# Kernel optimization log

Measured on AMD Instinct MI355X. Metric: run time of the kernel, lower is better.

Reference implementation:

```python
import jax, jax.numpy as jnp
import numpy as np

N, E, B = 51200, 819200, 64
F, G, GH, LH, LOUT = 64, 64, 128, 128, 1


def setup_inputs() -> dict:
    key = jax.random.key(0)
    ks = jax.random.split(key, 10)
    x = jax.random.normal(ks[0], (N, F), dtype=jnp.float32)
    e = jax.random.uniform(ks[1], (N, 1), dtype=jnp.float32)  # data.p[:, 0].view(-1, 1)
    edge_index = jax.random.randint(ks[2], (2, E), 0, N, dtype=jnp.int64)
    batch = jnp.sort(jax.random.randint(ks[3], (N,), 0, B, dtype=jnp.int64))

    def init_w(k, fan_in, fan_out):
        return (jax.random.normal(k, (fan_in, fan_out), dtype=jnp.float32)
                / np.float32(np.sqrt(fan_in)))

    # global PTConv nn: MLP(2F -> GH -> G)
    gW1 = init_w(ks[4], 2 * F, GH)
    gb1 = jnp.zeros((GH,), dtype=jnp.float32)
    gW2 = init_w(ks[5], GH, G)
    gb2 = jnp.zeros((G,), dtype=jnp.float32)
    # local PTConv nn: MLP(2*(F+G) -> LH -> 1)
    lW1 = init_w(ks[6], 2 * (F + G), LH)
    lb1 = jnp.zeros((LH,), dtype=jnp.float32)
    lW2 = init_w(ks[7], LH, LOUT)
    lb2 = jnp.zeros((LOUT,), dtype=jnp.float32)
    return {"x": x, "e": e, "edge_index": edge_index, "batch": batch,
            "gW1": gW1, "gb1": gb1, "gW2": gW2, "gb2": gb2,
            "lW1": lW1, "lb1": lb1, "lW2": lW2, "lb2": lb2}


def _mlp(h, W1, b1, W2, b2):
    return jax.nn.relu(h @ W1 + b1) @ W2 + b2


def _ptconv(x, edge_index, W1, b1, W2, b2, num_nodes):
    # PyG convention: edge_index[0]=src (j), edge_index[1]=dst (i); aggr='add'
    src, dst = edge_index[0], edge_index[1]
    h = jnp.concatenate([x[dst], x[src]], axis=-1)  # [E, 2*Fin] edge gather
    m = _mlp(h, W1, b1, W2, b2)                      # [E, Fout] edge MLP
    return jax.ops.segment_sum(m, dst, num_segments=num_nodes)  # scatter-add


def reference(x, e, edge_index, batch,
              gW1, gb1, gW2, gb2, lW1, lb1, lW2, lb2):
    n = x.shape[0]
    # EFNGlobal: PTConv -> energy weighting -> global_add_pool
    g = _ptconv(x, edge_index, gW1, gb1, gW2, gb2, n)   # [N, G]
    g = e * g                                           # e = p[:, 0:1]
    pooled = jax.ops.segment_sum(g, batch, num_segments=B)  # [B, G]
    # EFNLocal: broadcast per-graph scalars to nodes, concat, PTConv
    scalars = pooled[batch]                             # [N, G]
    xl = jnp.concatenate([x, scalars], axis=-1)         # [N, F+G]
    w_i = _ptconv(xl, edge_index, lW1, lb1, lW2, lb2, n)  # [N, 1]
    return w_i
```

## Files before the change

### kernel.cpp

```cpp
#include <hip/hip_runtime.h>
#include <hip/hip_bf16.h>

#define NN 51200
#define EE 819200
#define BB 64
#define NS 32
#define NPWG 4
#define NPWL 4
#define NBUCK 512
#define NPB 100
#define CAP 4096
#define EPB 4096

typedef __attribute__((ext_vector_type(8))) short short8;
typedef __attribute__((ext_vector_type(4))) float f32x4;

__device__ __forceinline__ ushort f2bf(float f) {
    unsigned int u = __float_as_uint(f);
    unsigned int r = (u + 0x7FFFu + ((u >> 16) & 1u)) >> 16;
    return (ushort)r;
}
__device__ __forceinline__ unsigned int cvt_pk_bf16(float lo, float hi) {
    unsigned int r;
    asm("v_cvt_pk_bf16_f32 %0, %1, %2" : "=v"(r) : "v"(lo), "v"(hi));
    return r;
}

__global__ void prep_weights(const float* __restrict__ gW1, const float* __restrict__ lW1,
                             ushort* __restrict__ W1p, ushort* __restrict__ L1p) {
    int tid = threadIdx.x;
    for (int idx = tid; idx < 64 * 256; idx += 512) {
        int i = idx & 7, c = (idx >> 3) & 255, q = idx >> 11;
        int k = (q >> 2) * 32 + (q & 3) * 8 + i;
        W1p[idx] = f2bf(c < 128 ? gW1[k * 128 + c] : gW1[(64 + k) * 128 + (c - 128)]);
        L1p[idx] = f2bf(c < 128 ? lW1[k * 128 + c] : lW1[(128 + k) * 128 + (c - 128)]);
    }
}

__global__ __launch_bounds__(512) void bucketA_kernel(const int* __restrict__ eidx,
                                                      int* __restrict__ bcnt,
                                                      int2* __restrict__ btmp) {
    __shared__ int2 sp[EPB];
    __shared__ ushort sb[EPB];
    __shared__ ushort perm[EPB];
    __shared__ int cnts[NBUCK];
    __shared__ int lofs[NBUCK];
    __shared__ int lcur[NBUCK];
    __shared__ int gbase[NBUCK];
    const int tid = threadIdx.x;
    const int base = blockIdx.x * EPB;

    cnts[tid] = 0;
    __syncthreads();
    for (int i = tid; i < EPB; i += 512) {
        int d = eidx[EE + base + i], s = eidx[base + i];
        sp[i] = make_int2(s, d);
        int b = d / NPB;
        sb[i] = (ushort)b;
        atomicAdd(&cnts[b], 1);
    }
    __syncthreads();
    const int v = cnts[tid];
    lofs[tid] = v;
    __syncthreads();
    for (int o = 1; o < NBUCK; o <<= 1) {
        int u = (tid >= o) ? lofs[tid - o] : 0;
        __syncthreads();
        lofs[tid] += u;
        __syncthreads();
    }
    const int excl = lofs[tid] - v;
    lofs[tid] = excl;
    lcur[tid] = excl;
    gbase[tid] = (v > 0) ? atomicAdd(&bcnt[tid * 16], v) : 0;
    __syncthreads();
    for (int i = tid; i < EPB; i += 512) {
        int pos = atomicAdd(&lcur[sb[i]], 1);
        perm[pos] = (ushort)i;
    }
    __syncthreads();
    {
        const int c = cnts[tid];
        const int lo = lofs[tid];
        int2* dst = btmp + (long)tid * CAP + gbase[tid];
        for (int j = 0; j < c; ++j) dst[j] = sp[perm[lo + j]];
    }
}

__global__ __launch_bounds__(512) void bucket_scan_kernel(const int* __restrict__ bcnt,
                                                          int* __restrict__ bbase) {
    __shared__ int s[NBUCK];
    const int t = threadIdx.x;
    int v = bcnt[t * 16];
    s[t] = v;
    __syncthreads();
    for (int o = 1; o < NBUCK; o <<= 1) {
        int u = (t >= o) ? s[t - o] : 0;
        __syncthreads();
        s[t] += u;
        __syncthreads();
    }
    bbase[t] = s[t] - v;
}

__global__ __launch_bounds__(256) void bucketB_kernel(const int2* __restrict__ btmp,
                                                      const int* __restrict__ bcnt,
                                                      const int* __restrict__ bbase,
                                                      int* __restrict__ offs,
                                                      int* __restrict__ csr) {
    __shared__ int lcnt[NPB];
    __shared__ int lofs[NPB];
    __shared__ int lcur[NPB];
    __shared__ int2 pairs[2048];
    const int bkt = blockIdx.x, tid = threadIdx.x;
    const int cnt = bcnt[bkt * 16];
    const int base = bbase[bkt];
    for (int j = tid; j < NPB; j += 256) lcnt[j] = 0;
    __syncthreads();
    for (int i = tid; i < cnt; i += 256) {
        int2 p = btmp[(long)bkt * CAP + i];
        if (i < 2048) pairs[i] = p;
        atomicAdd(&lcnt[p.y - bkt * NPB], 1);
    }
    __syncthreads();
    if (tid == 0) {
        int run = base;
        for (int j = 0; j < NPB; ++j) { lofs[j] = run; run += lcnt[j]; }
    }
    __syncthreads();
    for (int j = tid; j < NPB; j += 256) {
        lcur[j] = lofs[j];
        offs[bkt * NPB + j] = lofs[j];
    }
    if (bkt == NBUCK - 1 && tid == 0) offs[NN] = EE;
    __syncthreads();
    for (int i = tid; i < cnt; i += 256) {
        int2 p = (i < 2048) ? pairs[i] : btmp[(long)bkt * CAP + i];
        int pos = atomicAdd(&lcur[p.y - bkt * NPB], 1);
        csr[pos] = p.x;
    }
}

__global__ __launch_bounds__(512) void pq_gemm(
        const float* __restrict__ x, const ushort* __restrict__ Wp,
        const float* __restrict__ bias1, const float* __restrict__ T12,
        const int* __restrict__ batch, ushort* __restrict__ out) {
    const int tid = threadIdx.x;
    const int w = tid >> 6, l = tid & 63, lr = l & 15, lg = l >> 4;
    const int node = blockIdx.x * 128 + w * 16 + lr;

    short8 xa[2];
#pragma unroll
    for (int ks = 0; ks < 2; ++ks) {
        const float4* bp = reinterpret_cast<const float4*>(x + (long)node * 64 + ks * 32 + lg * 8);
        float4 f0 = bp[0], f1 = bp[1];
        union { short8 s; unsigned int u[4]; } t;
        t.u[0] = cvt_pk_bf16(f0.x, f0.y);
        t.u[1] = cvt_pk_bf16(f0.z, f0.w);
        t.u[2] = cvt_pk_bf16(f1.x, f1.y);
        t.u[3] = cvt_pk_bf16(f1.z, f1.w);
        xa[ks] = t.s;
    }
    f32x4 acc[16];
#pragma unroll
    for (int t = 0; t < 16; ++t)
#pragma unroll
        for (int i = 0; i < 4; ++i)
            acc[t][i] = (t < 8) ? bias1[t * 16 + lg * 4 + i] : 0.f;
#pragma unroll
    for (int ks = 0; ks < 2; ++ks)
#pragma unroll
        for (int t = 0; t < 16; ++t) {
            short8 wf = *reinterpret_cast<const short8*>(Wp + (((ks * 4 + lg) * 256) + t * 16 + lr) * 8);
            acc[t] = __builtin_amdgcn_mfma_f32_16x16x32_bf16(wf, xa[ks], acc[t], 0, 0, 0);
        }
    if (T12) {
        const float* tp = T12 + (long)batch[node] * 256;
#pragma unroll
        for (int t = 0; t < 16; ++t)
#pragma unroll
            for (int i = 0; i < 4; ++i)
                acc[t][i] += tp[t * 16 + lg * 4 + i];
    }
#pragma unroll
    for (int t = 0; t < 16; ++t) {
        uint2 v;
        v.x = cvt_pk_bf16(acc[t][0], acc[t][1]);
        v.y = cvt_pk_bf16(acc[t][2], acc[t][3]);
        *reinterpret_cast<uint2*>(out + (long)node * 256 + t * 16 + lg * 4) = v;
    }
}

__global__ __launch_bounds__(256) void global_edge(
        const ushort* __restrict__ PQ, const int* __restrict__ csr,
        const int* __restrict__ offs, const float* __restrict__ e,
        const int* __restrict__ batch,
        float* __restrict__ hidpart, float* __restrict__ esumpart) {
    const int tid = threadIdx.x;
    const int w = tid >> 6, l = tid & 63;
    const int wid = blockIdx.x * 4 + w;
    const int node0 = __builtin_amdgcn_readfirstlane(wid * NPWG);
    const int slot = wid & (NS - 1);

    float accp0 = 0.f, accp1 = 0.f, eacc = 0.f;
    int curb = batch[node0];

    for (int n = 0; n < NPWG; ++n) {
        const int node = node0 + n;
        const int off  = offs[node];
        const int cnt  = offs[node + 1] - off;
        const int bb   = batch[node];
        const float ev = e[node];
        if (bb != curb) {
            float* hp = hidpart + (long)slot * (BB * 128) + curb * 128;
            atomicAdd(hp + 2 * l, accp0);
            atomicAdd(hp + 2 * l + 1, accp1);
            if (l == 0) atomicAdd(&esumpart[slot * BB + curb], eacc);
            accp0 = accp1 = eacc = 0.f;
            curb = bb;
        }
        if (cnt <= 0) continue;
        const unsigned int pdu = *reinterpret_cast<const unsigned int*>(PQ + (long)node * 256 + 2 * l);
        const float p0 = __uint_as_float(pdu << 16);
        const float p1 = __uint_as_float(pdu & 0xFFFF0000u);
        float h0 = 0.f, h1 = 0.f;
        int g = 0;
        for (; g + 8 <= cnt; g += 8) {
            unsigned int qv[8];
#pragma unroll
            for (int k = 0; k < 8; ++k) {
                const int s = csr[off + g + k];
                qv[k] = *reinterpret_cast<const unsigned int*>(PQ + (long)s * 256 + 128 + 2 * l);
            }
#pragma unroll
            for (int k = 0; k < 8; ++k) {
                h0 += fmaxf(p0 + __uint_as_float(qv[k] << 16), 0.f);
                h1 += fmaxf(p1 + __uint_as_float(qv[k] & 0xFFFF0000u), 0.f);
            }
        }
        for (; g < cnt; ++g) {
            const int s = csr[off + g];
            const unsigned int qv = *reinterpret_cast<const unsigned int*>(PQ + (long)s * 256 + 128 + 2 * l);
            h0 += fmaxf(p0 + __uint_as_float(qv << 16), 0.f);
            h1 += fmaxf(p1 + __uint_as_float(qv & 0xFFFF0000u), 0.f);
        }
        accp0 += ev * h0; accp1 += ev * h1; eacc += ev * (float)cnt;
    }
    {
        float* hp = hidpart + (long)slot * (BB * 128) + curb * 128;
        atomicAdd(hp + 2 * l, accp0);
        atomicAdd(hp + 2 * l + 1, accp1);
        if (l == 0) atomicAdd(&esumpart[slot * BB + curb], eacc);
    }
}

__global__ __launch_bounds__(256) void pooled_t12_kernel(
        const float* __restrict__ hidpart, const float* __restrict__ esumpart,
        const float* __restrict__ gW2, const float* __restrict__ gb2,
        const float* __restrict__ lW1, float* __restrict__ T12) {
    __shared__ float hs[128];
    __shared__ float qacc[4][64];
    __shared__ float pb[64];
    __shared__ float esv;
    const int b = blockIdx.x, tid = threadIdx.x;
    if (tid < 128) {
        float s = 0.f;
        for (int sl = 0; sl < NS; ++sl) s += hidpart[(long)sl * (BB * 128) + b * 128 + tid];
        hs[tid] = s;
    } else if (tid == 128) {
        float s = 0.f;
        for (int sl = 0; sl < NS; ++sl) s += esumpart[sl * BB + b];
        esv = s;
    }
    __syncthreads();
    {
        int col = tid & 63, qr = tid >> 6;
        float a = 0.f;
        for (int k = qr * 32; k < qr * 32 + 32; ++k) a += hs[k] * gW2[k * 64 + col];
        qacc[qr][col] = a;
    }
    __syncthreads();
    if (tid < 64) pb[tid] = qacc[0][tid] + qacc[1][tid] + qacc[2][tid] + qacc[3][tid] + esv * gb2[tid];
    __syncthreads();
    const float* col = (tid < 128) ? (lW1 + 64 * 128 + tid) : (lW1 + 192 * 128 + (tid - 128));
    float acc = 0.f;
    for (int k = 0; k < 64; ++k) acc += pb[k] * col[k * 128];
    T12[b * 256 + tid] = acc;
}

__global__ __launch_bounds__(256) void local_edge(
        const ushort* __restrict__ PQL, const int* __restrict__ csr,
        const int* __restrict__ offs, const float* __restrict__ lW2,
        const float* __restrict__ lb2, float* __restrict__ out) {
    const int tid = threadIdx.x;
    const int w = tid >> 6, l = tid & 63;
    const int wid = blockIdx.x * 4 + w;
    const int node0 = __builtin_amdgcn_readfirstlane(wid * NPWL);
    const float w20 = lW2[2 * l], w21 = lW2[2 * l + 1];
    const float b2v = lb2[0];

    for (int n = 0; n < NPWL; ++n) {
        const int node = node0 + n;
        const int off = offs[node];
        const int cnt = offs[node + 1] - off;
        float dacc = 0.f;
        if (cnt > 0) {
            const unsigned int pdu = *reinterpret_cast<const unsigned int*>(PQL + (long)node * 256 + 2 * l);
            const float p0 = __uint_as_float(pdu << 16);
            const float p1 = __uint_as_float(pdu & 0xFFFF0000u);
            int g = 0;
            for (; g + 8 <= cnt; g += 8) {
                unsigned int qv[8];
#pragma unroll
                for (int k = 0; k < 8; ++k) {
                    const int s = csr[off + g + k];
                    qv[k] = *reinterpret_cast<const unsigned int*>(PQL + (long)s * 256 + 128 + 2 * l);
                }
#pragma unroll
                for (int k = 0; k < 8; ++k) {
                    dacc += fmaxf(p0 + __uint_as_float(qv[k] << 16), 0.f) * w20
                          + fmaxf(p1 + __uint_as_float(qv[k] & 0xFFFF0000u), 0.f) * w21;
                }
            }
            for (; g < cnt; ++g) {
                const int s = csr[off + g];
                const unsigned int qv = *reinterpret_cast<const unsigned int*>(PQL + (long)s * 256 + 128 + 2 * l);
                dacc += fmaxf(p0 + __uint_as_float(qv << 16), 0.f) * w20
                      + fmaxf(p1 + __uint_as_float(qv & 0xFFFF0000u), 0.f) * w21;
            }
            dacc += __shfl_xor(dacc, 1, 64);
            dacc += __shfl_xor(dacc, 2, 64);
            dacc += __shfl_xor(dacc, 4, 64);
            dacc += __shfl_xor(dacc, 8, 64);
            dacc += __shfl_xor(dacc, 16, 64);
            dacc += __shfl_xor(dacc, 32, 64);
        }
        if (l == 0) out[node] = dacc + (float)cnt * b2v;
    }
}

extern "C" void kernel_launch(void* const* d_in, const int* in_sizes, int n_in,
                              void* d_out, int out_size, void* d_ws, size_t ws_size,
                              hipStream_t stream) {
    const float* x   = (const float*)d_in[0];
    const float* e   = (const float*)d_in[1];
    const int*   ei  = (const int*)d_in[2];
    const int*   bat = (const int*)d_in[3];
    const float* gW1 = (const float*)d_in[4];
    const float* gb1 = (const float*)d_in[5];
    const float* gW2 = (const float*)d_in[6];
    const float* gb2 = (const float*)d_in[7];
    const float* lW1 = (const float*)d_in[8];
    const float* lb1 = (const float*)d_in[9];
    const float* lW2 = (const float*)d_in[10];
    const float* lb2 = (const float*)d_in[11];

    char* ws = (char*)d_ws;
    ushort* W1p     = (ushort*)(ws);
    ushort* L1p     = (ushort*)(ws + 32768);
    float*  T12     = (float*)(ws + 65536);
    float*  esumpart= (float*)(ws + 131072);
    float*  hidpart = (float*)(ws + 139264);
    int*    offs    = (int*)(ws + 1187840);
    int*    bcnt    = (int*)(ws + 1392672);
    int*    bbase   = (int*)(ws + 1425440);
    int*    csr     = (int*)(ws + 1427488);
    ushort* PQ      = (ushort*)(ws + 4704288);
    int2*   btmp    = (int2*)PQ;

    hipMemsetAsync(bcnt, 0, 32768, stream);
    hipMemsetAsync(esumpart, 0, 8192 + 1048576, stream);
    hipMemsetAsync(d_out, 0, (size_t)out_size * sizeof(float), stream);

    prep_weights<<<1, 512, 0, stream>>>(gW1, lW1, W1p, L1p);
    bucketA_kernel<<<EE / EPB, 512, 0, stream>>>(ei, bcnt, btmp);
    bucket_scan_kernel<<<1, NBUCK, 0, stream>>>(bcnt, bbase);
    bucketB_kernel<<<NBUCK, 256, 0, stream>>>(btmp, bcnt, bbase, offs, csr);

    pq_gemm<<<NN / 128, 512, 0, stream>>>(x, W1p, gb1, nullptr, bat, PQ);
    global_edge<<<NN / (4 * NPWG), 256, 0, stream>>>(PQ, csr, offs, e, bat, hidpart, esumpart);
    pooled_t12_kernel<<<BB, 256, 0, stream>>>(hidpart, esumpart, gW2, gb2, lW1, T12);
    pq_gemm<<<NN / 128, 512, 0, stream>>>(x, L1p, lb1, T12, bat, PQ);
    local_edge<<<NN / (4 * NPWL), 256, 0, stream>>>(PQ, csr, offs, lW2, lb2, (float*)d_out);
}
```

Before: 180.8 us.

## Partition CSR by source range and process edge ranges per 16-node group

The CSR build now also splits each destination bucket into four source-node ranges, producing a per-range offset table, and packs the local destination index into the upper bits of each CSR entry. Edge kernels launch one block per source range and node group and stream a contiguous edge range, switching destination on the fly and accumulating outputs with atomics. The goal is better cache locality for the gathered source rows (each block touches only a quarter of PQ) and even load balance across waves. The cost is extra atomics on outputs, per-edge branch checks, and a larger scan.

```diff
diff --git a/kernel.cpp b/kernel.cpp
--- a/kernel.cpp
+++ b/kernel.cpp
@@ -5,8 +5,8 @@
 #define EE 819200
 #define BB 64
 #define NS 32
-#define NPWG 4
-#define NPWL 4
+#define R4 4
+#define RSIZE 12800
 #define NBUCK 512
 #define NPB 100
 #define CAP 4096
@@ -25,6 +25,8 @@
     asm("v_cvt_pk_bf16_f32 %0, %1, %2" : "=v"(r) : "v"(lo), "v"(hi));
     return r;
 }
+__device__ __forceinline__ float blo(unsigned int q) { return __uint_as_float(q << 16); }
+__device__ __forceinline__ float bhi(unsigned int q) { return __uint_as_float(q & 0xFFFF0000u); }
 
 __global__ void prep_weights(const float* __restrict__ gW1, const float* __restrict__ lW1,
                              ushort* __restrict__ W1p, ushort* __restrict__ L1p) {
@@ -39,27 +41,28 @@
 
 __global__ __launch_bounds__(512) void bucketA_kernel(const int* __restrict__ eidx,
                                                       int* __restrict__ bcnt,
+                                                      int* __restrict__ cnt4,
                                                       int2* __restrict__ btmp) {
     __shared__ int2 sp[EPB];
-    __shared__ ushort sb[EPB];
     __shared__ ushort perm[EPB];
-    __shared__ int cnts[NBUCK];
-    __shared__ int lofs[NBUCK];
-    __shared__ int lcur[NBUCK];
-    __shared__ int gbase[NBUCK];
+    __shared__ int cnts[NBUCK], lofs[NBUCK], lcur[NBUCK];
+    __shared__ int c4[R4 * NBUCK];
     const int tid = threadIdx.x;
     const int base = blockIdx.x * EPB;
 
     cnts[tid] = 0;
+#pragma unroll
+    for (int j = 0; j < 4; ++j) c4[tid + j * 512] = 0;
     __syncthreads();
     for (int i = tid; i < EPB; i += 512) {
         int d = eidx[EE + base + i], s = eidx[base + i];
         sp[i] = make_int2(s, d);
-        int b = d / NPB;
-        sb[i] = (ushort)b;
-        atomicAdd(&cnts[b], 1);
-    }
-    __syncthreads();
+        atomicAdd(&cnts[d / NPB], 1);
+        atomicAdd(&c4[(s / RSIZE) * NBUCK + d / NPB], 1);
+    }
+    __syncthreads();
+    for (int j = tid; j < R4 * NBUCK; j += 512)
+        if (c4[j]) atomicAdd(&cnt4[j], c4[j]);
     const int v = cnts[tid];
     lofs[tid] = v;
     __syncthreads();
@@ -72,72 +75,77 @@
     const int excl = lofs[tid] - v;
     lofs[tid] = excl;
     lcur[tid] = excl;
-    gbase[tid] = (v > 0) ? atomicAdd(&bcnt[tid * 16], v) : 0;
+    const int mygbase = (v > 0) ? atomicAdd(&bcnt[tid * 16], v) : 0;
     __syncthreads();
     for (int i = tid; i < EPB; i += 512) {
-        int pos = atomicAdd(&lcur[sb[i]], 1);
+        int pos = atomicAdd(&lcur[sp[i].y / NPB], 1);
         perm[pos] = (ushort)i;
     }
     __syncthreads();
     {
         const int c = cnts[tid];
         const int lo = lofs[tid];
-        int2* dst = btmp + (long)tid * CAP + gbase[tid];
+        int2* dst = btmp + (long)tid * CAP + mygbase;
         for (int j = 0; j < c; ++j) dst[j] = sp[perm[lo + j]];
     }
 }
 
-__global__ __launch_bounds__(512) void bucket_scan_kernel(const int* __restrict__ bcnt,
-                                                          int* __restrict__ bbase) {
-    __shared__ int s[NBUCK];
+__global__ __launch_bounds__(512) void scan2048_kernel(const int* __restrict__ cnt4,
+                                                       int* __restrict__ base4,
+                                                       int* __restrict__ roffs4) {
+    __shared__ int s[512];
     const int t = threadIdx.x;
-    int v = bcnt[t * 16];
-    s[t] = v;
-    __syncthreads();
-    for (int o = 1; o < NBUCK; o <<= 1) {
+    int v0 = cnt4[t * 4], v1 = cnt4[t * 4 + 1], v2 = cnt4[t * 4 + 2], v3 = cnt4[t * 4 + 3];
+    int sum = v0 + v1 + v2 + v3;
+    s[t] = sum;
+    __syncthreads();
+    for (int o = 1; o < 512; o <<= 1) {
         int u = (t >= o) ? s[t - o] : 0;
         __syncthreads();
         s[t] += u;
         __syncthreads();
     }
-    bbase[t] = s[t] - v;
+    int run = s[t] - sum;
+    base4[t * 4] = run;
+    base4[t * 4 + 1] = run + v0;
+    base4[t * 4 + 2] = run + v0 + v1;
+    base4[t * 4 + 3] = run + v0 + v1 + v2;
+    if (t == 0) roffs4[R4 * NN] = EE;
 }
 
 __global__ __launch_bounds__(256) void bucketB_kernel(const int2* __restrict__ btmp,
                                                       const int* __restrict__ bcnt,
-                                                      const int* __restrict__ bbase,
-                                                      int* __restrict__ offs,
+                                                      const int* __restrict__ base4,
+                                                      int* __restrict__ roffs4,
                                                       int* __restrict__ csr) {
-    __shared__ int lcnt[NPB];
-    __shared__ int lofs[NPB];
-    __shared__ int lcur[NPB];
+    __shared__ int lcnt[R4 * NPB];
+    __shared__ int lcur[R4 * NPB];
     __shared__ int2 pairs[2048];
     const int bkt = blockIdx.x, tid = threadIdx.x;
     const int cnt = bcnt[bkt * 16];
-    const int base = bbase[bkt];
-    for (int j = tid; j < NPB; j += 256) lcnt[j] = 0;
+    for (int j = tid; j < R4 * NPB; j += 256) lcnt[j] = 0;
     __syncthreads();
     for (int i = tid; i < cnt; i += 256) {
         int2 p = btmp[(long)bkt * CAP + i];
         if (i < 2048) pairs[i] = p;
-        atomicAdd(&lcnt[p.y - bkt * NPB], 1);
-    }
-    __syncthreads();
-    if (tid == 0) {
-        int run = base;
-        for (int j = 0; j < NPB; ++j) { lofs[j] = run; run += lcnt[j]; }
-    }
-    __syncthreads();
-    for (int j = tid; j < NPB; j += 256) {
-        lcur[j] = lofs[j];
-        offs[bkt * NPB + j] = lofs[j];
-    }
-    if (bkt == NBUCK - 1 && tid == 0) offs[NN] = EE;
+        int key = (p.x / RSIZE) * NPB + (p.y - bkt * NPB);
+        atomicAdd(&lcnt[key], 1);
+    }
+    __syncthreads();
+    if (tid < R4) {
+        int run = base4[tid * NBUCK + bkt];
+        for (int nl = 0; nl < NPB; ++nl) {
+            roffs4[tid * NN + bkt * NPB + nl] = run;
+            lcur[tid * NPB + nl] = run;
+            run += lcnt[tid * NPB + nl];
+        }
+    }
     __syncthreads();
     for (int i = tid; i < cnt; i += 256) {
         int2 p = (i < 2048) ? pairs[i] : btmp[(long)bkt * CAP + i];
-        int pos = atomicAdd(&lcur[p.y - bkt * NPB], 1);
-        csr[pos] = p.x;
+        int key = (p.x / RSIZE) * NPB + (p.y - bkt * NPB);
+        int pos = atomicAdd(&lcur[key], 1);
+        csr[pos] = p.x | ((p.y & 15) << 17);
     }
 }
 
@@ -193,58 +201,79 @@
 
 __global__ __launch_bounds__(256) void global_edge(
         const ushort* __restrict__ PQ, const int* __restrict__ csr,
-        const int* __restrict__ offs, const float* __restrict__ e,
+        const int* __restrict__ roffs4, const float* __restrict__ e,
         const int* __restrict__ batch,
         float* __restrict__ hidpart, float* __restrict__ esumpart) {
-    const int tid = threadIdx.x;
-    const int w = tid >> 6, l = tid & 63;
-    const int wid = blockIdx.x * 4 + w;
-    const int node0 = __builtin_amdgcn_readfirstlane(wid * NPWG);
-    const int slot = wid & (NS - 1);
+    const int tid = threadIdx.x, w = tid >> 6, l = tid & 63;
+    const int rr = (blockIdx.x & 7) >> 1;
+    const int g  = (blockIdx.x >> 3) * 2 + (blockIdx.x & 1);
+    const int n0 = __builtin_amdgcn_readfirstlane(g * 64 + w * 16);
+    const int slot = (blockIdx.x * 4 + w) & (NS - 1);
+
+    int i = roffs4[rr * NN + n0];
+    const int iend = roffs4[rr * NN + n0 + 16];
 
     float accp0 = 0.f, accp1 = 0.f, eacc = 0.f;
-    int curb = batch[node0];
-
-    for (int n = 0; n < NPWG; ++n) {
-        const int node = node0 + n;
-        const int off  = offs[node];
-        const int cnt  = offs[node + 1] - off;
-        const int bb   = batch[node];
-        const float ev = e[node];
-        if (bb != curb) {
-            float* hp = hidpart + (long)slot * (BB * 128) + curb * 128;
-            atomicAdd(hp + 2 * l, accp0);
-            atomicAdd(hp + 2 * l + 1, accp1);
-            if (l == 0) atomicAdd(&esumpart[slot * BB + curb], eacc);
-            accp0 = accp1 = eacc = 0.f;
-            curb = bb;
-        }
-        if (cnt <= 0) continue;
-        const unsigned int pdu = *reinterpret_cast<const unsigned int*>(PQ + (long)node * 256 + 2 * l);
-        const float p0 = __uint_as_float(pdu << 16);
-        const float p1 = __uint_as_float(pdu & 0xFFFF0000u);
-        float h0 = 0.f, h1 = 0.f;
-        int g = 0;
-        for (; g + 8 <= cnt; g += 8) {
-            unsigned int qv[8];
-#pragma unroll
-            for (int k = 0; k < 8; ++k) {
-                const int s = csr[off + g + k];
-                qv[k] = *reinterpret_cast<const unsigned int*>(PQ + (long)s * 256 + 128 + 2 * l);
+    float p0 = 0.f, p1 = 0.f, ev = 0.f;
+    int curD = -1, curb = batch[n0];
+
+    for (; i + 8 <= iend; i += 8) {
+        int vv[8]; unsigned int qv[8];
+#pragma unroll
+        for (int k = 0; k < 8; ++k) vv[k] = csr[i + k];
+#pragma unroll
+        for (int k = 0; k < 8; ++k) {
+            const int s = vv[k] & 0x1FFFF;
+            qv[k] = *reinterpret_cast<const unsigned int*>(PQ + (long)s * 256 + 128 + 2 * l);
+        }
+#pragma unroll
+        for (int k = 0; k < 8; ++k) {
+            const int D = vv[k] >> 17;
+            if (D != curD) {
+                const int node = n0 + D;
+                const int bb = batch[node];
+                if (bb != curb) {
+                    float* hp = hidpart + (long)slot * (BB * 128) + curb * 128;
+                    atomicAdd(hp + 2 * l, accp0);
+                    atomicAdd(hp + 2 * l + 1, accp1);
+                    if (l == 0) atomicAdd(&esumpart[slot * BB + curb], eacc);
+                    accp0 = accp1 = eacc = 0.f;
+                    curb = bb;
+                }
+                const unsigned int pdu = *reinterpret_cast<const unsigned int*>(PQ + (long)node * 256 + 2 * l);
+                p0 = blo(pdu); p1 = bhi(pdu);
+                ev = e[node];
+                curD = D;
             }
-#pragma unroll
-            for (int k = 0; k < 8; ++k) {
-                h0 += fmaxf(p0 + __uint_as_float(qv[k] << 16), 0.f);
-                h1 += fmaxf(p1 + __uint_as_float(qv[k] & 0xFFFF0000u), 0.f);
+            accp0 += ev * fmaxf(p0 + blo(qv[k]), 0.f);
+            accp1 += ev * fmaxf(p1 + bhi(qv[k]), 0.f);
+            eacc += ev;
+        }
+    }
+    for (; i < iend; ++i) {
+        const int v = csr[i];
+        const int s = v & 0x1FFFF;
+        const unsigned int q = *reinterpret_cast<const unsigned int*>(PQ + (long)s * 256 + 128 + 2 * l);
+        const int D = v >> 17;
+        if (D != curD) {
+            const int node = n0 + D;
+            const int bb = batch[node];
+            if (bb != curb) {
+                float* hp = hidpart + (long)slot * (BB * 128) + curb * 128;
+                atomicAdd(hp + 2 * l, accp0);
+                atomicAdd(hp + 2 * l + 1, accp1);
+                if (l == 0) atomicAdd(&esumpart[slot * BB + curb], eacc);
+                accp0 = accp1 = eacc = 0.f;
+                curb = bb;
             }
-        }
-        for (; g < cnt; ++g) {
-            const int s = csr[off + g];
-            const unsigned int qv = *reinterpret_cast<const unsigned int*>(PQ + (long)s * 256 + 128 + 2 * l);
-            h0 += fmaxf(p0 + __uint_as_float(qv << 16), 0.f);
-            h1 += fmaxf(p1 + __uint_as_float(qv & 0xFFFF0000u), 0.f);
-        }
-        accp0 += ev * h0; accp1 += ev * h1; eacc += ev * (float)cnt;
+            const unsigned int pdu = *reinterpret_cast<const unsigned int*>(PQ + (long)node * 256 + 2 * l);
+            p0 = blo(pdu); p1 = bhi(pdu);
+            ev = e[node];
+            curD = D;
+        }
+        accp0 += ev * fmaxf(p0 + blo(q), 0.f);
+        accp1 += ev * fmaxf(p1 + bhi(q), 0.f);
+        eacc += ev;
     }
     {
         float* hp = hidpart + (long)slot * (BB * 128) + curb * 128;
@@ -290,52 +319,77 @@
 
 __global__ __launch_bounds__(256) void local_edge(
         const ushort* __restrict__ PQL, const int* __restrict__ csr,
-        const int* __restrict__ offs, const float* __restrict__ lW2,
+        const int* __restrict__ roffs4, const float* __restrict__ lW2,
         const float* __restrict__ lb2, float* __restrict__ out) {
-    const int tid = threadIdx.x;
-    const int w = tid >> 6, l = tid & 63;
-    const int wid = blockIdx.x * 4 + w;
-    const int node0 = __builtin_amdgcn_readfirstlane(wid * NPWL);
+    const int tid = threadIdx.x, w = tid >> 6, l = tid & 63;
+    const int rr = (blockIdx.x & 7) >> 1;
+    const int g  = (blockIdx.x >> 3) * 2 + (blockIdx.x & 1);
+    const int n0 = __builtin_amdgcn_readfirstlane(g * 64 + w * 16);
     const float w20 = lW2[2 * l], w21 = lW2[2 * l + 1];
     const float b2v = lb2[0];
 
-    for (int n = 0; n < NPWL; ++n) {
-        const int node = node0 + n;
-        const int off = offs[node];
-        const int cnt = offs[node + 1] - off;
-        float dacc = 0.f;
-        if (cnt > 0) {
-            const unsigned int pdu = *reinterpret_cast<const unsigned int*>(PQL + (long)node * 256 + 2 * l);
-            const float p0 = __uint_as_float(pdu << 16);
-            const float p1 = __uint_as_float(pdu & 0xFFFF0000u);
-            int g = 0;
-            for (; g + 8 <= cnt; g += 8) {
-                unsigned int qv[8];
-#pragma unroll
-                for (int k = 0; k < 8; ++k) {
-                    const int s = csr[off + g + k];
-                    qv[k] = *reinterpret_cast<const unsigned int*>(PQL + (long)s * 256 + 128 + 2 * l);
+    int i = roffs4[rr * NN + n0];
+    const int iend = roffs4[rr * NN + n0 + 16];
+
+    float dacc = 0.f, p0 = 0.f, p1 = 0.f;
+    int curD = -1, ecnt = 0;
+
+    for (; i + 8 <= iend; i += 8) {
+        int vv[8]; unsigned int qv[8];
+#pragma unroll
+        for (int k = 0; k < 8; ++k) vv[k] = csr[i + k];
+#pragma unroll
+        for (int k = 0; k < 8; ++k) {
+            const int s = vv[k] & 0x1FFFF;
+            qv[k] = *reinterpret_cast<const unsigned int*>(PQL + (long)s * 256 + 128 + 2 * l);
+        }
+#pragma unroll
+        for (int k = 0; k < 8; ++k) {
+            const int D = vv[k] >> 17;
+            if (D != curD) {
+                if (curD >= 0) {
+                    float r = dacc;
+                    r += __shfl_xor(r, 1, 64);  r += __shfl_xor(r, 2, 64);
+                    r += __shfl_xor(r, 4, 64);  r += __shfl_xor(r, 8, 64);
+                    r += __shfl_xor(r, 16, 64); r += __shfl_xor(r, 32, 64);
+                    if (l == 0) atomicAdd(&out[n0 + curD], r + (float)ecnt * b2v);
                 }
-#pragma unroll
-                for (int k = 0; k < 8; ++k) {
-                    dacc += fmaxf(p0 + __uint_as_float(qv[k] << 16), 0.f) * w20
-                          + fmaxf(p1 + __uint_as_float(qv[k] & 0xFFFF0000u), 0.f) * w21;
-                }
+                dacc = 0.f; ecnt = 0;
+                const unsigned int pdu = *reinterpret_cast<const unsigned int*>(PQL + (long)(n0 + D) * 256 + 2 * l);
+                p0 = blo(pdu); p1 = bhi(pdu);
+                curD = D;
             }
-            for (; g < cnt; ++g) {
-                const int s = csr[off + g];
-                const unsigned int qv = *reinterpret_cast<const unsigned int*>(PQL + (long)s * 256 + 128 + 2 * l);
-                dacc += fmaxf(p0 + __uint_as_float(qv << 16), 0.f) * w20
-                      + fmaxf(p1 + __uint_as_float(qv & 0xFFFF0000u), 0.f) * w21;
+            dacc += fmaxf(p0 + blo(qv[k]), 0.f) * w20 + fmaxf(p1 + bhi(qv[k]), 0.f) * w21;
+            ecnt++;
+        }
+    }
+    for (; i < iend; ++i) {
+        const int v = csr[i];
+        const int s = v & 0x1FFFF;
+        const unsigned int q = *reinterpret_cast<const unsigned int*>(PQL + (long)s * 256 + 128 + 2 * l);
+        const int D = v >> 17;
+        if (D != curD) {
+            if (curD >= 0) {
+                float r = dacc;
+                r += __shfl_xor(r, 1, 64);  r += __shfl_xor(r, 2, 64);
+                r += __shfl_xor(r, 4, 64);  r += __shfl_xor(r, 8, 64);
+                r += __shfl_xor(r, 16, 64); r += __shfl_xor(r, 32, 64);
+                if (l == 0) atomicAdd(&out[n0 + curD], r + (float)ecnt * b2v);
             }
-            dacc += __shfl_xor(dacc, 1, 64);
-            dacc += __shfl_xor(dacc, 2, 64);
-            dacc += __shfl_xor(dacc, 4, 64);
-            dacc += __shfl_xor(dacc, 8, 64);
-            dacc += __shfl_xor(dacc, 16, 64);
-            dacc += __shfl_xor(dacc, 32, 64);
-        }
-        if (l == 0) out[node] = dacc + (float)cnt * b2v;
+            dacc = 0.f; ecnt = 0;
+            const unsigned int pdu = *reinterpret_cast<const unsigned int*>(PQL + (long)(n0 + D) * 256 + 2 * l);
+            p0 = blo(pdu); p1 = bhi(pdu);
+            curD = D;
+        }
+        dacc += fmaxf(p0 + blo(q), 0.f) * w20 + fmaxf(p1 + bhi(q), 0.f) * w21;
+        ecnt++;
+    }
+    if (curD >= 0) {
+        float r = dacc;
+        r += __shfl_xor(r, 1, 64);  r += __shfl_xor(r, 2, 64);
+        r += __shfl_xor(r, 4, 64);  r += __shfl_xor(r, 8, 64);
+        r += __shfl_xor(r, 16, 64); r += __shfl_xor(r, 32, 64);
+        if (l == 0) atomicAdd(&out[n0 + curD], r + (float)ecnt * b2v);
     }
 }
 
@@ -361,25 +415,26 @@
     float*  T12     = (float*)(ws + 65536);
     float*  esumpart= (float*)(ws + 131072);
     float*  hidpart = (float*)(ws + 139264);
-    int*    offs    = (int*)(ws + 1187840);
-    int*    bcnt    = (int*)(ws + 1392672);
-    int*    bbase   = (int*)(ws + 1425440);
-    int*    csr     = (int*)(ws + 1427488);
-    ushort* PQ      = (ushort*)(ws + 4704288);
+    int*    roffs4  = (int*)(ws + 1187840);
+    int*    bcnt    = (int*)(ws + 2007044);
+    int*    cnt4    = (int*)(ws + 2039812);
+    int*    base4   = (int*)(ws + 2048004);
+    int*    csr     = (int*)(ws + 2056196);
+    ushort* PQ      = (ushort*)(ws + 5333008);
     int2*   btmp    = (int2*)PQ;
 
-    hipMemsetAsync(bcnt, 0, 32768, stream);
+    hipMemsetAsync(bcnt, 0, 32768 + 8192, stream);
     hipMemsetAsync(esumpart, 0, 8192 + 1048576, stream);
     hipMemsetAsync(d_out, 0, (size_t)out_size * sizeof(float), stream);
 
     prep_weights<<<1, 512, 0, stream>>>(gW1, lW1, W1p, L1p);
-    bucketA_kernel<<<EE / EPB, 512, 0, stream>>>(ei, bcnt, btmp);
-    bucket_scan_kernel<<<1, NBUCK, 0, stream>>>(bcnt, bbase);
-    bucketB_kernel<<<NBUCK, 256, 0, stream>>>(btmp, bcnt, bbase, offs, csr);
+    bucketA_kernel<<<EE / EPB, 512, 0, stream>>>(ei, bcnt, cnt4, btmp);
+    scan2048_kernel<<<1, 512, 0, stream>>>(cnt4, base4, roffs4);
+    bucketB_kernel<<<NBUCK, 256, 0, stream>>>(btmp, bcnt, base4, roffs4, csr);
 
     pq_gemm<<<NN / 128, 512, 0, stream>>>(x, W1p, gb1, nullptr, bat, PQ);
-    global_edge<<<NN / (4 * NPWG), 256, 0, stream>>>(PQ, csr, offs, e, bat, hidpart, esumpart);
+    global_edge<<<(NN / 64) * R4, 256, 0, stream>>>(PQ, csr, roffs4, e, bat, hidpart, esumpart);
     pooled_t12_kernel<<<BB, 256, 0, stream>>>(hidpart, esumpart, gW2, gb2, lW1, T12);
     pq_gemm<<<NN / 128, 512, 0, stream>>>(x, L1p, lb1, T12, bat, PQ);
-    local_edge<<<NN / (4 * NPWL), 256, 0, stream>>>(PQ, csr, offs, lW2, lb2, (float*)d_out);
-}
+    local_edge<<<(NN / 64) * R4, 256, 0, stream>>>(PQ, csr, roffs4, lW2, lb2, (float*)d_out);
+}
```

Result: slower. 185.3 us (+2.5%).

## Split wavefront into half-waves processing two edges each with 8-byte gathers

Applied to the files above, without the earlier changes.

In global_edge and local_edge, each wave now splits into two 32-lane halves. Each half gathers a different source edge's 128-wide bf16 row, with each lane loading 8 bytes (4 features) instead of 4 bytes. The two halves are combined by an xor-shuffle before the atomics or the final reduction. This halves the number of gather iterations per edge and widens each load, in exchange for an odd-edge tail with masked work and an extra cross-half shuffle. A minor change keeps the bucket global base in a register instead of shared memory.

```diff
diff --git a/kernel.cpp b/kernel.cpp
--- a/kernel.cpp
+++ b/kernel.cpp
@@ -25,6 +25,8 @@
     asm("v_cvt_pk_bf16_f32 %0, %1, %2" : "=v"(r) : "v"(lo), "v"(hi));
     return r;
 }
+__device__ __forceinline__ float blo(unsigned int q) { return __uint_as_float(q << 16); }
+__device__ __forceinline__ float bhi(unsigned int q) { return __uint_as_float(q & 0xFFFF0000u); }
 
 __global__ void prep_weights(const float* __restrict__ gW1, const float* __restrict__ lW1,
                              ushort* __restrict__ W1p, ushort* __restrict__ L1p) {
@@ -46,7 +48,6 @@
     __shared__ int cnts[NBUCK];
     __shared__ int lofs[NBUCK];
     __shared__ int lcur[NBUCK];
-    __shared__ int gbase[NBUCK];
     const int tid = threadIdx.x;
     const int base = blockIdx.x * EPB;
 
@@ -72,7 +73,7 @@
     const int excl = lofs[tid] - v;
     lofs[tid] = excl;
     lcur[tid] = excl;
-    gbase[tid] = (v > 0) ? atomicAdd(&bcnt[tid * 16], v) : 0;
+    const int mygbase = (v > 0) ? atomicAdd(&bcnt[tid * 16], v) : 0;
     __syncthreads();
     for (int i = tid; i < EPB; i += 512) {
         int pos = atomicAdd(&lcur[sb[i]], 1);
@@ -82,7 +83,7 @@
     {
         const int c = cnts[tid];
         const int lo = lofs[tid];
-        int2* dst = btmp + (long)tid * CAP + gbase[tid];
+        int2* dst = btmp + (long)tid * CAP + mygbase;
         for (int j = 0; j < c; ++j) dst[j] = sp[perm[lo + j]];
     }
 }
@@ -197,12 +198,14 @@
         const int* __restrict__ batch,
         float* __restrict__ hidpart, float* __restrict__ esumpart) {
     const int tid = threadIdx.x;
-    const int w = tid >> 6, l = tid & 63;
+    const int w = tid >> 6, l = tid & 63, c = l & 31;
+    const bool hi = l >= 32;
     const int wid = blockIdx.x * 4 + w;
     const int node0 = __builtin_amdgcn_readfirstlane(wid * NPWG);
     const int slot = wid & (NS - 1);
 
-    float accp0 = 0.f, accp1 = 0.f, eacc = 0.f;
+    float accp[4] = {0.f, 0.f, 0.f, 0.f};
+    float eacc = 0.f;
     int curb = batch[node0];
 
     for (int n = 0; n < NPWG; ++n) {
@@ -212,44 +215,71 @@
         const int bb   = batch[node];
         const float ev = e[node];
         if (bb != curb) {
-            float* hp = hidpart + (long)slot * (BB * 128) + curb * 128;
-            atomicAdd(hp + 2 * l, accp0);
-            atomicAdd(hp + 2 * l + 1, accp1);
+#pragma unroll
+            for (int j = 0; j < 4; ++j) accp[j] += __shfl_xor(accp[j], 32, 64);
+            float* hp = hidpart + (long)slot * (BB * 128) + curb * 128 + 4 * c;
+            if (!hi) {
+#pragma unroll
+                for (int j = 0; j < 4; ++j) atomicAdd(hp + j, accp[j]);
+            }
             if (l == 0) atomicAdd(&esumpart[slot * BB + curb], eacc);
-            accp0 = accp1 = eacc = 0.f;
+#pragma unroll
+            for (int j = 0; j < 4; ++j) accp[j] = 0.f;
+            eacc = 0.f;
             curb = bb;
         }
         if (cnt <= 0) continue;
-        const unsigned int pdu = *reinterpret_cast<const unsigned int*>(PQ + (long)node * 256 + 2 * l);
-        const float p0 = __uint_as_float(pdu << 16);
-        const float p1 = __uint_as_float(pdu & 0xFFFF0000u);
-        float h0 = 0.f, h1 = 0.f;
+        const uint2 pdu = *reinterpret_cast<const uint2*>(PQ + (long)node * 256 + 4 * c);
+        const float pv0 = blo(pdu.x), pv1 = bhi(pdu.x), pv2 = blo(pdu.y), pv3 = bhi(pdu.y);
+        float h0 = 0.f, h1 = 0.f, h2 = 0.f, h3 = 0.f;
         int g = 0;
-        for (; g + 8 <= cnt; g += 8) {
-            unsigned int qv[8];
+        for (; g + 16 <= cnt; g += 16) {
+            uint2 qv[8];
 #pragma unroll
             for (int k = 0; k < 8; ++k) {
-                const int s = csr[off + g + k];
-                qv[k] = *reinterpret_cast<const unsigned int*>(PQ + (long)s * 256 + 128 + 2 * l);
+                const int sa = csr[off + g + 2 * k];
+                const int sb = csr[off + g + 2 * k + 1];
+                const int s = hi ? sb : sa;
+                qv[k] = *reinterpret_cast<const uint2*>(PQ + (long)s * 256 + 128 + 4 * c);
             }
 #pragma unroll
             for (int k = 0; k < 8; ++k) {
-                h0 += fmaxf(p0 + __uint_as_float(qv[k] << 16), 0.f);
-                h1 += fmaxf(p1 + __uint_as_float(qv[k] & 0xFFFF0000u), 0.f);
-            }
-        }
-        for (; g < cnt; ++g) {
+                h0 += fmaxf(pv0 + blo(qv[k].x), 0.f);
+                h1 += fmaxf(pv1 + bhi(qv[k].x), 0.f);
+                h2 += fmaxf(pv2 + blo(qv[k].y), 0.f);
+                h3 += fmaxf(pv3 + bhi(qv[k].y), 0.f);
+            }
+        }
+        for (; g + 2 <= cnt; g += 2) {
+            const int sa = csr[off + g], sb = csr[off + g + 1];
+            const int s = hi ? sb : sa;
+            const uint2 q = *reinterpret_cast<const uint2*>(PQ + (long)s * 256 + 128 + 4 * c);
+            h0 += fmaxf(pv0 + blo(q.x), 0.f);
+            h1 += fmaxf(pv1 + bhi(q.x), 0.f);
+            h2 += fmaxf(pv2 + blo(q.y), 0.f);
+            h3 += fmaxf(pv3 + bhi(q.y), 0.f);
+        }
+        if (g < cnt) {
             const int s = csr[off + g];
-            const unsigned int qv = *reinterpret_cast<const unsigned int*>(PQ + (long)s * 256 + 128 + 2 * l);
-            h0 += fmaxf(p0 + __uint_as_float(qv << 16), 0.f);
-            h1 += fmaxf(p1 + __uint_as_float(qv & 0xFFFF0000u), 0.f);
-        }
-        accp0 += ev * h0; accp1 += ev * h1; eacc += ev * (float)cnt;
+            const uint2 q = *reinterpret_cast<const uint2*>(PQ + (long)s * 256 + 128 + 4 * c);
+            if (!hi) {
+                h0 += fmaxf(pv0 + blo(q.x), 0.f);
+                h1 += fmaxf(pv1 + bhi(q.x), 0.f);
+                h2 += fmaxf(pv2 + blo(q.y), 0.f);
+                h3 += fmaxf(pv3 + bhi(q.y), 0.f);
+            }
+        }
+        accp[0] += ev * h0; accp[1] += ev * h1; accp[2] += ev * h2; accp[3] += ev * h3;
+        eacc += ev * (float)cnt;
     }
     {
-        float* hp = hidpart + (long)slot * (BB * 128) + curb * 128;
-        atomicAdd(hp + 2 * l, accp0);
-        atomicAdd(hp + 2 * l + 1, accp1);
+#pragma unroll
+        for (int j = 0; j < 4; ++j) accp[j] += __shfl_xor(accp[j], 32, 64);
+        float* hp = hidpart + (long)slot * (BB * 128) + curb * 128 + 4 * c;
+        if (!hi) {
+#pragma unroll
+            for (int j = 0; j < 4; ++j) atomicAdd(hp + j, accp[j]);
+        }
         if (l == 0) atomicAdd(&esumpart[slot * BB + curb], eacc);
     }
 }
@@ -293,10 +323,11 @@
         const int* __restrict__ offs, const float* __restrict__ lW2,
         const float* __restrict__ lb2, float* __restrict__ out) {
     const int tid = threadIdx.x;
-    const int w = tid >> 6, l = tid & 63;
+    const int w = tid >> 6, l = tid & 63, c = l & 31;
+    const bool hi = l >= 32;
     const int wid = blockIdx.x * 4 + w;
     const int node0 = __builtin_amdgcn_readfirstlane(wid * NPWL);
-    const float w20 = lW2[2 * l], w21 = lW2[2 * l + 1];
+    const float4 w4 = *reinterpret_cast<const float4*>(lW2 + 4 * c);
     const float b2v = lb2[0];
 
     for (int n = 0; n < NPWL; ++n) {
@@ -305,28 +336,44 @@
         const int cnt = offs[node + 1] - off;
         float dacc = 0.f;
         if (cnt > 0) {
-            const unsigned int pdu = *reinterpret_cast<const unsigned int*>(PQL + (long)node * 256 + 2 * l);
-            const float p0 = __uint_as_float(pdu << 16);
-            const float p1 = __uint_as_float(pdu & 0xFFFF0000u);
+            const uint2 pdu = *reinterpret_cast<const uint2*>(PQL + (long)node * 256 + 4 * c);
+            const float pv0 = blo(pdu.x), pv1 = bhi(pdu.x), pv2 = blo(pdu.y), pv3 = bhi(pdu.y);
             int g = 0;
-            for (; g + 8 <= cnt; g += 8) {
-                unsigned int qv[8];
+            for (; g + 16 <= cnt; g += 16) {
+                uint2 qv[8];
 #pragma unroll
                 for (int k = 0; k < 8; ++k) {
-                    const int s = csr[off + g + k];
-                    qv[k] = *reinterpret_cast<const unsigned int*>(PQL + (long)s * 256 + 128 + 2 * l);
+                    const int sa = csr[off + g + 2 * k];
+                    const int sb = csr[off + g + 2 * k + 1];
+                    const int s = hi ? sb : sa;
+                    qv[k] = *reinterpret_cast<const uint2*>(PQL + (long)s * 256 + 128 + 4 * c);
                 }
 #pragma unroll
                 for (int k = 0; k < 8; ++k) {
-                    dacc += fmaxf(p0 + __uint_as_float(qv[k] << 16), 0.f) * w20
-                          + fmaxf(p1 + __uint_as_float(qv[k] & 0xFFFF0000u), 0.f) * w21;
+                    dacc += fmaxf(pv0 + blo(qv[k].x), 0.f) * w4.x
+                          + fmaxf(pv1 + bhi(qv[k].x), 0.f) * w4.y
+                          + fmaxf(pv2 + blo(qv[k].y), 0.f) * w4.z
+                          + fmaxf(pv3 + bhi(qv[k].y), 0.f) * w4.w;
                 }
             }
-            for (; g < cnt; ++g) {
+            for (; g + 2 <= cnt; g += 2) {
+                const int sa = csr[off + g], sb = csr[off + g + 1];
+                const int s = hi ? sb : sa;
+                const uint2 q = *reinterpret_cast<const uint2*>(PQL + (long)s * 256 + 128 + 4 * c);
+                dacc += fmaxf(pv0 + blo(q.x), 0.f) * w4.x
+                      + fmaxf(pv1 + bhi(q.x), 0.f) * w4.y
+                      + fmaxf(pv2 + blo(q.y), 0.f) * w4.z
+                      + fmaxf(pv3 + bhi(q.y), 0.f) * w4.w;
+            }
+            if (g < cnt) {
                 const int s = csr[off + g];
-                const unsigned int qv = *reinterpret_cast<const unsigned int*>(PQL + (long)s * 256 + 128 + 2 * l);
-                dacc += fmaxf(p0 + __uint_as_float(qv << 16), 0.f) * w20
-                      + fmaxf(p1 + __uint_as_float(qv & 0xFFFF0000u), 0.f) * w21;
+                const uint2 q = *reinterpret_cast<const uint2*>(PQL + (long)s * 256 + 128 + 4 * c);
+                if (!hi) {
+                    dacc += fmaxf(pv0 + blo(q.x), 0.f) * w4.x
+                          + fmaxf(pv1 + bhi(q.x), 0.f) * w4.y
+                          + fmaxf(pv2 + blo(q.y), 0.f) * w4.z
+                          + fmaxf(pv3 + bhi(q.y), 0.f) * w4.w;
+                }
             }
             dacc += __shfl_xor(dacc, 1, 64);
             dacc += __shfl_xor(dacc, 2, 64);
```

New measurement: 193.0 us. 6.8% more time.
